# Performance work log

Hardware: AMD Instinct MI355X
Metric: run time of the kernel (lower is better)

Reference implementation:

```python
import jax, jax.numpy as jnp
import numpy as np

HEADS = 8


def setup_inputs() -> dict:
    key = jax.random.key(0)
    ks = jax.random.split(key, 5)
    B, C, H, W = 2, 256, 48, 48
    s = 0.02
    return {
        "ct": jax.random.normal(ks[0], (B, C, H, W), jnp.float32),
        "us": jax.random.normal(ks[1], (B, C, H, W), jnp.float32),
        "w_qkv_ct": jax.random.normal(ks[2], (3 * C, C), jnp.float32) * s,
        "w_qkv_us": jax.random.normal(ks[3], (3 * C, C), jnp.float32) * s,
        "w_proj": jax.random.normal(ks[4], (C, 2 * C), jnp.float32) * s,
        "b_proj": jnp.zeros((C,), jnp.float32),
    }


def _heads_view(x, B, H, W):
    # [B, C, H, W] -> [B, heads, HW, dh]
    C = x.shape[1]
    return x.reshape(B, HEADS, C // HEADS, H * W).transpose(0, 1, 3, 2)


def _cross_attn(q, k, v, scale):
    # q,k,v: [B, heads, HW, dh]
    attn = jax.nn.softmax(jnp.einsum("bhnd,bhmd->bhnm", q, k) * scale, axis=-1)
    return jnp.einsum("bhnm,bhmd->bhnd", attn, v)


def reference(ct, us, w_qkv_ct, w_qkv_us, w_proj, b_proj):
    B, C, H, W = ct.shape
    dh = C // HEADS
    scale = dh ** (-0.5)

    # 1x1 convs as channel GEMMs
    qkv1 = jnp.einsum("oc,bchw->bohw", w_qkv_ct, ct)
    qkv2 = jnp.einsum("oc,bchw->bohw", w_qkv_us, us)
    q1, k1, v1 = jnp.split(qkv1, 3, axis=1)
    q2, k2, v2 = jnp.split(qkv2, 3, axis=1)

    # CT queries attend to US keys/values
    o1 = _cross_attn(_heads_view(q1, B, H, W), _heads_view(k2, B, H, W),
                     _heads_view(v2, B, H, W), scale)
    # US queries attend to CT keys/values
    o2 = _cross_attn(_heads_view(q2, B, H, W), _heads_view(k1, B, H, W),
                     _heads_view(v1, B, H, W), scale)

    # [B, heads, HW, dh] -> [B, C, H, W]
    out1 = o1.transpose(0, 1, 3, 2).reshape(B, C, H, W)
    out2 = o2.transpose(0, 1, 3, 2).reshape(B, C, H, W)

    fused = jnp.concatenate([ct + out1, us + out2], axis=1)
    return jnp.einsum("oc,bchw->bohw", w_proj, fused) + b_proj[None, :, None, None]
```

## Files before the change

### kernel.cpp

```cpp
#include <hip/hip_runtime.h>
#include <hip/hip_bf16.h>
#include <math.h>

#define HW   2304
#define CCH  256

#define QSCALE 0.25504368686637270f

typedef short short8 __attribute__((ext_vector_type(8)));
typedef float f32x4  __attribute__((ext_vector_type(4)));

__device__ inline unsigned short f2bf(float f) {
    union { float f; unsigned u; } v; v.f = f;
    unsigned r = v.u + 0x7FFF + ((v.u >> 16) & 1);
    return (unsigned short)(r >> 16);
}
__device__ inline unsigned pkbf2(float a, float b) {
    float2 f; f.x = a; f.y = b;
    union { __hip_bfloat162 h; unsigned u; } c;
    c.h = __float22bfloat162_rn(f);
    return c.u;
}
__device__ inline unsigned pktrunc(float a, float b) {
    return __builtin_amdgcn_perm(__builtin_bit_cast(unsigned, b),
                                 __builtin_bit_cast(unsigned, a), 0x07060302u);
}


__device__ __forceinline__ void prep_unit(
    int u, int t,
    const float* __restrict__ ct, const float* __restrict__ us,
    const float* __restrict__ w1, const float* __restrict__ w2,
    const float* __restrict__ w3,
    unsigned short* __restrict__ xT,
    unsigned short* __restrict__ wb1, unsigned short* __restrict__ wb2,
    unsigned short* __restrict__ w3b,
    unsigned short* __restrict__ Ts )
{
    if (u >= 576) {
        const int v_ = u - 576;
        int z, base;
        if (v_ < 192)      { z = 0; base = v_ * 1024; }
        else if (v_ < 384) { z = 1; base = (v_ - 192) * 1024; }
        else               { z = 2; base = (v_ - 384) * 1024; }
        const float* s = (z == 0) ? w1 : (z == 1) ? w2 : w3;
        unsigned short* d = (z == 0) ? wb1 : (z == 1) ? wb2 : w3b;
        const int i = base + t * 4;
        const float4 v4 = *(const float4*)&s[i];
        const float sc = (z < 2 && i < 65536) ? QSCALE : 1.f;
        uint2 p; p.x = pkbf2(v4.x * sc, v4.y * sc); p.y = pkbf2(v4.z * sc, v4.w * sc);
        *(uint2*)&d[i] = p;
        return;
    }
    const int pt = u % 36, rest = u / 36, ctile = rest & 3, z = rest >> 2;
    const float* __restrict__ src = ((z >> 1) ? us : ct) + (size_t)(z & 1) * CCH * HW;
    unsigned short* __restrict__ dst = xT + (size_t)z * HW * 256;
    const int p0 = pt * 64, c0 = ctile * 64;
    const int m = t & 15, ms = (m & 7) << 3;
    __syncthreads();
#pragma unroll
    for (int r = 0; r < 4; r++) {
        const int c = (t >> 4) + 16 * r;
        const float4 v4 = *(const float4*)&src[(size_t)(c0 + c) * HW + p0 + m * 4];
        const int cs = c ^ ms;
        Ts[(m * 4 + 0) * 72 + cs] = f2bf(v4.x);
        Ts[(m * 4 + 1) * 72 + cs] = f2bf(v4.y);
        Ts[(m * 4 + 2) * 72 + cs] = f2bf(v4.z);
        Ts[(m * 4 + 3) * 72 + cs] = f2bf(v4.w);
    }
    __syncthreads();
    const int p = t >> 2, c8 = (t & 3) * 16;
    const int es = ((p >> 2) & 7) << 3;
    const short8 a  = *(const short8*)&Ts[p * 72 + (c8 ^ es)];
    const short8 b8 = *(const short8*)&Ts[p * 72 + ((c8 + 8) ^ es)];
    *(short8*)&dst[(size_t)(p0 + p) * 256 + c0 + c8]     = a;
    *(short8*)&dst[(size_t)(p0 + p) * 256 + c0 + c8 + 8] = b8;
}

__device__ __forceinline__ void qkv_unit(
    int ptile, int otile, int z, int t,
    const unsigned short* __restrict__ xT,
    const unsigned short* __restrict__ wb1, const unsigned short* __restrict__ wb2,
    unsigned short* __restrict__ qkvT1, unsigned short* __restrict__ qkvT2,
    unsigned short* __restrict__ vdm1,  unsigned short* __restrict__ vdm2,
    unsigned short* __restrict__ Ws, unsigned short* __restrict__ Xs)
{
    const int inp = z >> 1, b = z & 1;
    const unsigned short* __restrict__ X = xT + (size_t)(inp * 2 + b) * HW * 256;
    const unsigned short* __restrict__ W = inp ? wb2 : wb1;
    unsigned short* __restrict__ qT = (inp ? qkvT2 : qkvT1) + (size_t)b * HW * 512;
    unsigned short* __restrict__ vd = (inp ? vdm2 : vdm1) + (size_t)b * CCH * HW;
    const int p0 = ptile * 64, o0 = otile * 64;
    const int w = t >> 6, lane = t & 63, quad = lane >> 4, m = lane & 15;
    const int sr = t >> 3, sc = t & 7;

    f32x4 acc[4] = {{0,0,0,0},{0,0,0,0},{0,0,0,0},{0,0,0,0}};

    short8 wv0 = *(const short8*)&W[(size_t)(o0 + sr) * 256 + sc * 8];
    short8 wv1 = *(const short8*)&W[(size_t)(o0 + 32 + sr) * 256 + sc * 8];
    short8 xv0 = *(const short8*)&X[(size_t)(p0 + sr) * 256 + sc * 8];
    short8 xv1 = *(const short8*)&X[(size_t)(p0 + 32 + sr) * 256 + sc * 8];

    for (int k0 = 0; k0 < 256; k0 += 64) {
        __syncthreads();
        *(short8*)&Ws[sr * 72 + sc * 8] = wv0;
        *(short8*)&Ws[(32 + sr) * 72 + sc * 8] = wv1;
        *(short8*)&Xs[sr * 72 + sc * 8] = xv0;
        *(short8*)&Xs[(32 + sr) * 72 + sc * 8] = xv1;
        __syncthreads();
        const int kn = k0 + 64;
        if (kn < 256) {
            wv0 = *(const short8*)&W[(size_t)(o0 + sr) * 256 + kn + sc * 8];
            wv1 = *(const short8*)&W[(size_t)(o0 + 32 + sr) * 256 + kn + sc * 8];
            xv0 = *(const short8*)&X[(size_t)(p0 + sr) * 256 + kn + sc * 8];
            xv1 = *(const short8*)&X[(size_t)(p0 + 32 + sr) * 256 + kn + sc * 8];
        }
#pragma unroll
        for (int kc2 = 0; kc2 < 2; kc2++) {
            const short8 af = *(const short8*)&Ws[(w * 16 + m) * 72 + kc2 * 32 + quad * 8];
#pragma unroll
            for (int pg = 0; pg < 4; pg++) {
                const short8 bf = *(const short8*)&Xs[(pg * 16 + m) * 72 + kc2 * 32 + quad * 8];
                acc[pg] = __builtin_amdgcn_mfma_f32_16x16x32_bf16(af, bf, acc[pg], 0, 0, 0);
            }
        }
    }
    __syncthreads();
    if (o0 < 512) {
#pragma unroll
        for (int pg = 0; pg < 4; pg++) {
            uint2 pk; pk.x = pkbf2(acc[pg][0], acc[pg][1]); pk.y = pkbf2(acc[pg][2], acc[pg][3]);
            *(uint2*)&Ws[(pg * 16 + m) * 72 + w * 16 + quad * 4] = pk;
        }
        __syncthreads();
        const int pr = t >> 2, cc = t & 3;
        const uint4 d0 = *(const uint4*)&Ws[pr * 72 + cc * 16];
        const uint4 d1 = *(const uint4*)&Ws[pr * 72 + cc * 16 + 8];
        *(uint4*)&qT[(size_t)(p0 + pr) * 512 + o0 + cc * 16]     = d0;
        *(uint4*)&qT[(size_t)(p0 + pr) * 512 + o0 + cc * 16 + 8] = d1;
    } else {
#pragma unroll
        for (int pg = 0; pg < 4; pg++)
#pragma unroll
            for (int r = 0; r < 4; r++)
                Ws[(w * 16 + quad * 4 + r) * 72 + pg * 16 + m] = f2bf(acc[pg][r]);
        __syncthreads();
        const int dr = t >> 2, cc = t & 3;
        const uint4 d0 = *(const uint4*)&Ws[dr * 72 + cc * 16];
        const uint4 d1 = *(const uint4*)&Ws[dr * 72 + cc * 16 + 8];
        *(uint4*)&vd[(size_t)(o0 - 512 + dr) * HW + p0 + cc * 16]     = d0;
        *(uint4*)&vd[(size_t)(o0 - 512 + dr) * HW + p0 + cc * 16 + 8] = d1;
    }
    __syncthreads();
}

__device__ __forceinline__ void attn_unit(
    int ptile, int dir, int b, int h, int t,
    const unsigned short* __restrict__ qkvT1, const unsigned short* __restrict__ qkvT2,
    const unsigned short* __restrict__ vdm1,  const unsigned short* __restrict__ vdm2,
    const float* __restrict__ ct, const float* __restrict__ us,
    unsigned short* __restrict__ fusedT,
    unsigned short* __restrict__ Ks , unsigned short* __restrict__ Vs )
{
    const unsigned short* __restrict__ Qt = (dir ? qkvT2 : qkvT1) + (size_t)b * HW * 512;
    const unsigned short* __restrict__ Kt = (dir ? qkvT1 : qkvT2) + (size_t)b * HW * 512
                                            + 256 + h * 32;
    const unsigned short* __restrict__ Vd = (dir ? vdm1 : vdm2) + ((size_t)b * CCH + h * 32) * HW;
    const float* __restrict__ src = (dir ? us : ct) + ((size_t)b * CCH + h * 32) * HW;

    const int w = t >> 6, lane = t & 63, quad = lane >> 4, m = lane & 15;
    const int kj0 = t >> 2, kcs = t & 3;
    const int pcK = kcs ^ (((kj0 >> 1) & 1) | (((kj0 >> 3) & 1) << 1));
    const int vr0 = t >> 4, vcs = t & 15;
    const int g2m = ((m >> 1) & 1) | (((m >> 2) & 1) << 1);
    const unsigned short* __restrict__ ksb =
        &Ks[((m >> 2) * 8 + (m & 3)) * 32 + (quad ^ g2m) * 8];
    const unsigned short* __restrict__ vsb = &Vs[m * 136 + quad * 8];
    const short ONE = (short)0x3F80;
    const short8 ones = {ONE,ONE,ONE,ONE,ONE,ONE,ONE,ONE};

    const int pqA = ptile * 128 + w * 32 + m;
    const short8 qfA = *(const short8*)&Qt[(size_t)pqA * 512 + h * 32 + quad * 8];
    const short8 qfB = *(const short8*)&Qt[(size_t)(pqA + 16) * 512 + h * 32 + quad * 8];

    f32x4 acc0A = {0,0,0,0}, acc1A = {0,0,0,0}, acclA = {0,0,0,0};
    f32x4 acc0B = {0,0,0,0}, acc1B = {0,0,0,0}, acclB = {0,0,0,0};

    short8 ka = *(const short8*)&Kt[(size_t)kj0 * 512 + kcs * 8];
    short8 kb = *(const short8*)&Kt[(size_t)(kj0 + 64) * 512 + kcs * 8];
    short8 va = *(const short8*)&Vd[(size_t)vr0 * HW + vcs * 8];
    short8 vb = *(const short8*)&Vd[(size_t)(vr0 + 16) * HW + vcs * 8];

    for (int j0 = 0; j0 < HW; j0 += 128) {
        __syncthreads();
        *(short8*)&Ks[kj0 * 32 + pcK * 8] = ka;
        *(short8*)&Ks[(kj0 + 64) * 32 + pcK * 8] = kb;
        *(short8*)&Vs[vr0 * 136 + vcs * 8] = va;
        *(short8*)&Vs[(vr0 + 16) * 136 + vcs * 8] = vb;
        __syncthreads();

        const int jn = j0 + 128;
        if (jn < HW) {
            ka = *(const short8*)&Kt[(size_t)(jn + kj0) * 512 + kcs * 8];
            kb = *(const short8*)&Kt[(size_t)(jn + kj0 + 64) * 512 + kcs * 8];
            va = *(const short8*)&Vd[(size_t)vr0 * HW + jn + vcs * 8];
            vb = *(const short8*)&Vd[(size_t)(vr0 + 16) * HW + jn + vcs * 8];
        }

        uint4 pwA[4], pwB[4];
#pragma unroll
        for (int f = 0; f < 8; f++) {
            const short8 kf = *(const short8*)(ksb + ((f >> 1) * 32 + (f & 1) * 4) * 32);
            const f32x4 z = {0,0,0,0};
            const f32x4 SA = __builtin_amdgcn_mfma_f32_16x16x32_bf16(kf, qfA, z, 0, 0, 0);
            const f32x4 SB = __builtin_amdgcn_mfma_f32_16x16x32_bf16(kf, qfB, z, 0, 0, 0);
            const float a0 = __builtin_amdgcn_exp2f(SA[0]);
            const float a1 = __builtin_amdgcn_exp2f(SA[1]);
            const float a2 = __builtin_amdgcn_exp2f(SA[2]);
            const float a3 = __builtin_amdgcn_exp2f(SA[3]);
            const float b0 = __builtin_amdgcn_exp2f(SB[0]);
            const float b1 = __builtin_amdgcn_exp2f(SB[1]);
            const float b2 = __builtin_amdgcn_exp2f(SB[2]);
            const float b3 = __builtin_amdgcn_exp2f(SB[3]);
            if ((f & 1) == 0) {
                pwA[f >> 1].x = pktrunc(a0, a1); pwA[f >> 1].y = pktrunc(a2, a3);
                pwB[f >> 1].x = pktrunc(b0, b1); pwB[f >> 1].y = pktrunc(b2, b3);
            } else {
                pwA[f >> 1].z = pktrunc(a0, a1); pwA[f >> 1].w = pktrunc(a2, a3);
                pwB[f >> 1].z = pktrunc(b0, b1); pwB[f >> 1].w = pktrunc(b2, b3);
            }
        }
#pragma unroll
        for (int kt = 0; kt < 4; kt++) {
            const short8 pfA = __builtin_bit_cast(short8, pwA[kt]);
            const short8 pfB = __builtin_bit_cast(short8, pwB[kt]);
            const short8 vf0 = *(const short8*)(vsb + kt * 32);
            const short8 vf1 = *(const short8*)(vsb + 16 * 136 + kt * 32);
            acc0A = __builtin_amdgcn_mfma_f32_16x16x32_bf16(vf0, pfA, acc0A, 0, 0, 0);
            acc1A = __builtin_amdgcn_mfma_f32_16x16x32_bf16(vf1, pfA, acc1A, 0, 0, 0);
            acclA = __builtin_amdgcn_mfma_f32_16x16x32_bf16(ones, pfA, acclA, 0, 0, 0);
            acc0B = __builtin_amdgcn_mfma_f32_16x16x32_bf16(vf0, pfB, acc0B, 0, 0, 0);
            acc1B = __builtin_amdgcn_mfma_f32_16x16x32_bf16(vf1, pfB, acc1B, 0, 0, 0);
            acclB = __builtin_amdgcn_mfma_f32_16x16x32_bf16(ones, pfB, acclB, 0, 0, 0);
        }
    }

    const int cb = dir * 256 + h * 32, d0 = quad * 4;
    {
        const float inv = 1.f / acclA[0];
        unsigned short* __restrict__ fT = fusedT + ((size_t)b * HW + pqA) * 512 + cb + d0;
        uint2 s0, s1;
        s0.x = pkbf2(acc0A[0] * inv + src[(size_t)(d0 + 0) * HW + pqA],
                     acc0A[1] * inv + src[(size_t)(d0 + 1) * HW + pqA]);
        s0.y = pkbf2(acc0A[2] * inv + src[(size_t)(d0 + 2) * HW + pqA],
                     acc0A[3] * inv + src[(size_t)(d0 + 3) * HW + pqA]);
        s1.x = pkbf2(acc1A[0] * inv + src[(size_t)(16 + d0 + 0) * HW + pqA],
                     acc1A[1] * inv + src[(size_t)(16 + d0 + 1) * HW + pqA]);
        s1.y = pkbf2(acc1A[2] * inv + src[(size_t)(16 + d0 + 2) * HW + pqA],
                     acc1A[3] * inv + src[(size_t)(16 + d0 + 3) * HW + pqA]);
        *(uint2*)&fT[0]  = s0;
        *(uint2*)&fT[16] = s1;
    }
    {
        const int pqB = pqA + 16;
        const float inv = 1.f / acclB[0];
        unsigned short* __restrict__ fT = fusedT + ((size_t)b * HW + pqB) * 512 + cb + d0;
        uint2 s0, s1;
        s0.x = pkbf2(acc0B[0] * inv + src[(size_t)(d0 + 0) * HW + pqB],
                     acc0B[1] * inv + src[(size_t)(d0 + 1) * HW + pqB]);
        s0.y = pkbf2(acc0B[2] * inv + src[(size_t)(d0 + 2) * HW + pqB],
                     acc0B[3] * inv + src[(size_t)(d0 + 3) * HW + pqB]);
        s1.x = pkbf2(acc1B[0] * inv + src[(size_t)(16 + d0 + 0) * HW + pqB],
                     acc1B[1] * inv + src[(size_t)(16 + d0 + 1) * HW + pqB]);
        s1.y = pkbf2(acc1B[2] * inv + src[(size_t)(16 + d0 + 2) * HW + pqB],
                     acc1B[3] * inv + src[(size_t)(16 + d0 + 3) * HW + pqB]);
        *(uint2*)&fT[0]  = s0;
        *(uint2*)&fT[16] = s1;
    }
    __syncthreads();
}

__device__ __forceinline__ void proj_unit(
    int ptile, int otile, int t,
    const unsigned short* __restrict__ w3b, const unsigned short* __restrict__ fusedT,
    const float* __restrict__ bias, float* __restrict__ out,
    unsigned short* __restrict__ Ws, unsigned short* __restrict__ Xs)
{
    const int p0 = ptile * 64, o0 = otile * 64;
    const int w = t >> 6, lane = t & 63, quad = lane >> 4, m = lane & 15;
    const int sr = t >> 3, sc = t & 7;

    f32x4 acc[4] = {{0,0,0,0},{0,0,0,0},{0,0,0,0},{0,0,0,0}};

    short8 wv0 = *(const short8*)&w3b[(size_t)(o0 + sr) * 512 + sc * 8];
    short8 wv1 = *(const short8*)&w3b[(size_t)(o0 + 32 + sr) * 512 + sc * 8];
    short8 xv0 = *(const short8*)&fusedT[(size_t)(p0 + sr) * 512 + sc * 8];
    short8 xv1 = *(const short8*)&fusedT[(size_t)(p0 + 32 + sr) * 512 + sc * 8];

    for (int k0 = 0; k0 < 512; k0 += 64) {
        __syncthreads();
        *(short8*)&Ws[sr * 72 + sc * 8] = wv0;
        *(short8*)&Ws[(32 + sr) * 72 + sc * 8] = wv1;
        *(short8*)&Xs[sr * 72 + sc * 8] = xv0;
        *(short8*)&Xs[(32 + sr) * 72 + sc * 8] = xv1;
        __syncthreads();
        const int kn = k0 + 64;
        if (kn < 512) {
            wv0 = *(const short8*)&w3b[(size_t)(o0 + sr) * 512 + kn + sc * 8];
            wv1 = *(const short8*)&w3b[(size_t)(o0 + 32 + sr) * 512 + kn + sc * 8];
            xv0 = *(const short8*)&fusedT[(size_t)(p0 + sr) * 512 + kn + sc * 8];
            xv1 = *(const short8*)&fusedT[(size_t)(p0 + 32 + sr) * 512 + kn + sc * 8];
        }
#pragma unroll
        for (int kc2 = 0; kc2 < 2; kc2++) {
            const short8 af = *(const short8*)&Ws[(w * 16 + m) * 72 + kc2 * 32 + quad * 8];
#pragma unroll
            for (int pg = 0; pg < 4; pg++) {
                const short8 bf = *(const short8*)&Xs[(pg * 16 + m) * 72 + kc2 * 32 + quad * 8];
                acc[pg] = __builtin_amdgcn_mfma_f32_16x16x32_bf16(af, bf, acc[pg], 0, 0, 0);
            }
        }
    }
    const int b = (p0 >= HW) ? 1 : 0;
    const int pl0 = p0 - b * HW;
    float* __restrict__ ob = out + (size_t)b * CCH * HW;
    float b4[4];
#pragma unroll
    for (int r = 0; r < 4; r++) b4[r] = bias[o0 + w * 16 + quad * 4 + r];
#pragma unroll
    for (int pg = 0; pg < 4; pg++)
#pragma unroll
        for (int r = 0; r < 4; r++)
            ob[(size_t)(o0 + w * 16 + quad * 4 + r) * HW + pl0 + pg * 16 + m]
                = acc[pg][r] + b4[r];
}

__global__ __launch_bounds__(256, 4) void prep_k(
    const float* __restrict__ ct, const float* __restrict__ us,
    const float* __restrict__ w1, const float* __restrict__ w2,
    const float* __restrict__ w3,
    unsigned short* __restrict__ xT,
    unsigned short* __restrict__ b1, unsigned short* __restrict__ b2,
    unsigned short* __restrict__ b3)
{
    __shared__ __align__(16) unsigned short Ts[64 * 72];
    prep_unit(blockIdx.x, threadIdx.x, ct, us, w1, w2, w3, xT, b1, b2, b3, Ts);
}

__global__ __launch_bounds__(256, 4) void qkv_k(
    const unsigned short* __restrict__ xT,
    const unsigned short* __restrict__ wb1, const unsigned short* __restrict__ wb2,
    unsigned short* __restrict__ qkvT1, unsigned short* __restrict__ qkvT2,
    unsigned short* __restrict__ vdm1,  unsigned short* __restrict__ vdm2)
{
    __shared__ __align__(16) unsigned short Ws[64 * 72];
    __shared__ __align__(16) unsigned short Xs[64 * 72];
    qkv_unit(blockIdx.x, blockIdx.y, blockIdx.z, threadIdx.x,
             xT, wb1, wb2, qkvT1, qkvT2, vdm1, vdm2, Ws, Xs);
}

__global__ __launch_bounds__(256, 3) void attn_k(
    const unsigned short* __restrict__ qkvT1, const unsigned short* __restrict__ qkvT2,
    const unsigned short* __restrict__ vdm1,  const unsigned short* __restrict__ vdm2,
    const float* __restrict__ ct, const float* __restrict__ us,
    unsigned short* __restrict__ fusedT)
{
    __shared__ __align__(16) unsigned short Ks[128 * 32];
    __shared__ __align__(16) unsigned short Vs[32 * 136];
    attn_unit(blockIdx.x, blockIdx.z, blockIdx.y >> 3, blockIdx.y & 7, threadIdx.x,
              qkvT1, qkvT2, vdm1, vdm2, ct, us, fusedT, Ks, Vs);
}

__global__ __launch_bounds__(256, 4) void proj_k(
    const unsigned short* __restrict__ w3b, const unsigned short* __restrict__ fusedT,
    const float* __restrict__ bias, float* __restrict__ out)
{
    __shared__ __align__(16) unsigned short Ws[64 * 72];
    __shared__ __align__(16) unsigned short Xs[64 * 72];
    proj_unit(blockIdx.x, blockIdx.y, threadIdx.x, w3b, fusedT, bias, out, Ws, Xs);
}

extern "C" void kernel_launch(void* const* d_in, const int* in_sizes, int n_in,
                              void* d_out, int out_size, void* d_ws, size_t ws_size,
                              hipStream_t stream)
{
    const float* ct       = (const float*)d_in[0];
    const float* us       = (const float*)d_in[1];
    const float* w_qkv_ct = (const float*)d_in[2];
    const float* w_qkv_us = (const float*)d_in[3];
    const float* w_proj   = (const float*)d_in[4];
    const float* b_proj   = (const float*)d_in[5];
    float* out = (float*)d_out;

    unsigned short* wb1   = (unsigned short*)d_ws;
    unsigned short* wb2   = wb1 + (size_t)768 * 256;
    unsigned short* w3b   = wb2 + (size_t)768 * 256;
    unsigned short* xT    = w3b + (size_t)256 * 512;
    unsigned short* qkvT1 = xT    + (size_t)4 * HW * 256;
    unsigned short* qkvT2 = qkvT1 + (size_t)2 * HW * 512;
    unsigned short* vdm1  = qkvT2 + (size_t)2 * HW * 512;
    unsigned short* vdm2  = vdm1  + (size_t)2 * CCH * HW;
    unsigned short* fusedT= vdm2  + (size_t)2 * CCH * HW;

    prep_k<<<dim3(1088), 256, 0, stream>>>(ct, us, w_qkv_ct, w_qkv_us, w_proj,
                                           xT, wb1, wb2, w3b);
    qkv_k <<<dim3(36, 12, 4), 256, 0, stream>>>(xT, wb1, wb2, qkvT1, qkvT2, vdm1, vdm2);
    attn_k<<<dim3(18, 16, 2), 256, 0, stream>>>(qkvT1, qkvT2, vdm1, vdm2, ct, us, fusedT);
    proj_k<<<dim3(72, 4), 256, 0, stream>>>(w3b, fusedT, b_proj, out);
}
```

Measured before the change: 125.4 us.

## Double-buffer K/V tiles in attention and fix prep transpose swizzle

The attention kernel now keeps two LDS buffers for the K and V tiles. The next tile is written into the spare buffer while the current one is consumed, which cuts the loop from two barriers per iteration to one. The attention launch-bounds occupancy hint rises from 3 to 4 blocks per CU. The transpose in the prep kernel gets a changed XOR swizzle to reduce LDS bank conflicts. The extra buffer doubles attention LDS use, and the higher occupancy target may add register pressure or spills.

```diff
diff --git a/kernel.cpp b/kernel.cpp
--- a/kernel.cpp
+++ b/kernel.cpp
@@ -56,7 +56,7 @@
     const float* __restrict__ src = ((z >> 1) ? us : ct) + (size_t)(z & 1) * CCH * HW;
     unsigned short* __restrict__ dst = xT + (size_t)z * HW * 256;
     const int p0 = pt * 64, c0 = ctile * 64;
-    const int m = t & 15, ms = (m & 7) << 3;
+    const int m = t & 15, ms = ((m >> 1) & 7) << 3;
     __syncthreads();
 #pragma unroll
     for (int r = 0; r < 4; r++) {
@@ -70,7 +70,7 @@
     }
     __syncthreads();
     const int p = t >> 2, c8 = (t & 3) * 16;
-    const int es = ((p >> 2) & 7) << 3;
+    const int es = ((p >> 3) & 7) << 3;
     const short8 a  = *(const short8*)&Ts[p * 72 + (c8 ^ es)];
     const short8 b8 = *(const short8*)&Ts[p * 72 + ((c8 + 8) ^ es)];
     *(short8*)&dst[(size_t)(p0 + p) * 256 + c0 + c8]     = a;
@@ -154,14 +154,98 @@
     __syncthreads();
 }
 
-__device__ __forceinline__ void attn_unit(
-    int ptile, int dir, int b, int h, int t,
+__device__ __forceinline__ void proj_unit(
+    int ptile, int otile, int t,
+    const unsigned short* __restrict__ w3b, const unsigned short* __restrict__ fusedT,
+    const float* __restrict__ bias, float* __restrict__ out,
+    unsigned short* __restrict__ Ws, unsigned short* __restrict__ Xs)
+{
+    const int p0 = ptile * 64, o0 = otile * 64;
+    const int w = t >> 6, lane = t & 63, quad = lane >> 4, m = lane & 15;
+    const int sr = t >> 3, sc = t & 7;
+
+    f32x4 acc[4] = {{0,0,0,0},{0,0,0,0},{0,0,0,0},{0,0,0,0}};
+
+    short8 wv0 = *(const short8*)&w3b[(size_t)(o0 + sr) * 512 + sc * 8];
+    short8 wv1 = *(const short8*)&w3b[(size_t)(o0 + 32 + sr) * 512 + sc * 8];
+    short8 xv0 = *(const short8*)&fusedT[(size_t)(p0 + sr) * 512 + sc * 8];
+    short8 xv1 = *(const short8*)&fusedT[(size_t)(p0 + 32 + sr) * 512 + sc * 8];
+
+    for (int k0 = 0; k0 < 512; k0 += 64) {
+        __syncthreads();
+        *(short8*)&Ws[sr * 72 + sc * 8] = wv0;
+        *(short8*)&Ws[(32 + sr) * 72 + sc * 8] = wv1;
+        *(short8*)&Xs[sr * 72 + sc * 8] = xv0;
+        *(short8*)&Xs[(32 + sr) * 72 + sc * 8] = xv1;
+        __syncthreads();
+        const int kn = k0 + 64;
+        if (kn < 512) {
+            wv0 = *(const short8*)&w3b[(size_t)(o0 + sr) * 512 + kn + sc * 8];
+            wv1 = *(const short8*)&w3b[(size_t)(o0 + 32 + sr) * 512 + kn + sc * 8];
+            xv0 = *(const short8*)&fusedT[(size_t)(p0 + sr) * 512 + kn + sc * 8];
+            xv1 = *(const short8*)&fusedT[(size_t)(p0 + 32 + sr) * 512 + kn + sc * 8];
+        }
+#pragma unroll
+        for (int kc2 = 0; kc2 < 2; kc2++) {
+            const short8 af = *(const short8*)&Ws[(w * 16 + m) * 72 + kc2 * 32 + quad * 8];
+#pragma unroll
+            for (int pg = 0; pg < 4; pg++) {
+                const short8 bf = *(const short8*)&Xs[(pg * 16 + m) * 72 + kc2 * 32 + quad * 8];
+                acc[pg] = __builtin_amdgcn_mfma_f32_16x16x32_bf16(af, bf, acc[pg], 0, 0, 0);
+            }
+        }
+    }
+    const int b = (p0 >= HW) ? 1 : 0;
+    const int pl0 = p0 - b * HW;
+    float* __restrict__ ob = out + (size_t)b * CCH * HW;
+    float b4[4];
+#pragma unroll
+    for (int r = 0; r < 4; r++) b4[r] = bias[o0 + w * 16 + quad * 4 + r];
+#pragma unroll
+    for (int pg = 0; pg < 4; pg++)
+#pragma unroll
+        for (int r = 0; r < 4; r++)
+            ob[(size_t)(o0 + w * 16 + quad * 4 + r) * HW + pl0 + pg * 16 + m]
+                = acc[pg][r] + b4[r];
+}
+
+__global__ __launch_bounds__(256, 4) void prep_k(
+    const float* __restrict__ ct, const float* __restrict__ us,
+    const float* __restrict__ w1, const float* __restrict__ w2,
+    const float* __restrict__ w3,
+    unsigned short* __restrict__ xT,
+    unsigned short* __restrict__ b1, unsigned short* __restrict__ b2,
+    unsigned short* __restrict__ b3)
+{
+    __shared__ __align__(16) unsigned short Ts[64 * 72];
+    prep_unit(blockIdx.x, threadIdx.x, ct, us, w1, w2, w3, xT, b1, b2, b3, Ts);
+}
+
+__global__ __launch_bounds__(256, 4) void qkv_k(
+    const unsigned short* __restrict__ xT,
+    const unsigned short* __restrict__ wb1, const unsigned short* __restrict__ wb2,
+    unsigned short* __restrict__ qkvT1, unsigned short* __restrict__ qkvT2,
+    unsigned short* __restrict__ vdm1,  unsigned short* __restrict__ vdm2)
+{
+    __shared__ __align__(16) unsigned short Ws[64 * 72];
+    __shared__ __align__(16) unsigned short Xs[64 * 72];
+    qkv_unit(blockIdx.x, blockIdx.y, blockIdx.z, threadIdx.x,
+             xT, wb1, wb2, qkvT1, qkvT2, vdm1, vdm2, Ws, Xs);
+}
+
+__global__ __launch_bounds__(256, 4) void attn_k(
     const unsigned short* __restrict__ qkvT1, const unsigned short* __restrict__ qkvT2,
     const unsigned short* __restrict__ vdm1,  const unsigned short* __restrict__ vdm2,
     const float* __restrict__ ct, const float* __restrict__ us,
-    unsigned short* __restrict__ fusedT,
-    unsigned short* __restrict__ Ks , unsigned short* __restrict__ Vs )
-{
+    unsigned short* __restrict__ fusedT)
+{
+    __shared__ __align__(16) unsigned short Ks[2][128 * 32];
+    __shared__ __align__(16) unsigned short Vs[2][32 * 136];
+    const int t = threadIdx.x;
+
+    const int ptile = blockIdx.x, dir = blockIdx.z;
+    const int b = blockIdx.y >> 3, h = blockIdx.y & 7;
+
     const unsigned short* __restrict__ Qt = (dir ? qkvT2 : qkvT1) + (size_t)b * HW * 512;
     const unsigned short* __restrict__ Kt = (dir ? qkvT1 : qkvT2) + (size_t)b * HW * 512
                                             + 256 + h * 32;
@@ -173,9 +257,8 @@
     const int pcK = kcs ^ (((kj0 >> 1) & 1) | (((kj0 >> 3) & 1) << 1));
     const int vr0 = t >> 4, vcs = t & 15;
     const int g2m = ((m >> 1) & 1) | (((m >> 2) & 1) << 1);
-    const unsigned short* __restrict__ ksb =
-        &Ks[((m >> 2) * 8 + (m & 3)) * 32 + (quad ^ g2m) * 8];
-    const unsigned short* __restrict__ vsb = &Vs[m * 136 + quad * 8];
+    const int ksb_off = ((m >> 2) * 8 + (m & 3)) * 32 + (quad ^ g2m) * 8;
+    const int vsb_off = m * 136 + quad * 8;
     const short ONE = (short)0x3F80;
     const short8 ones = {ONE,ONE,ONE,ONE,ONE,ONE,ONE,ONE};
 
@@ -190,22 +273,34 @@
     short8 kb = *(const short8*)&Kt[(size_t)(kj0 + 64) * 512 + kcs * 8];
     short8 va = *(const short8*)&Vd[(size_t)vr0 * HW + vcs * 8];
     short8 vb = *(const short8*)&Vd[(size_t)(vr0 + 16) * HW + vcs * 8];
-
-    for (int j0 = 0; j0 < HW; j0 += 128) {
-        __syncthreads();
-        *(short8*)&Ks[kj0 * 32 + pcK * 8] = ka;
-        *(short8*)&Ks[(kj0 + 64) * 32 + pcK * 8] = kb;
-        *(short8*)&Vs[vr0 * 136 + vcs * 8] = va;
-        *(short8*)&Vs[(vr0 + 16) * 136 + vcs * 8] = vb;
-        __syncthreads();
-
-        const int jn = j0 + 128;
+    *(short8*)&Ks[0][kj0 * 32 + pcK * 8] = ka;
+    *(short8*)&Ks[0][(kj0 + 64) * 32 + pcK * 8] = kb;
+    *(short8*)&Vs[0][vr0 * 136 + vcs * 8] = va;
+    *(short8*)&Vs[0][(vr0 + 16) * 136 + vcs * 8] = vb;
+    ka = *(const short8*)&Kt[(size_t)(128 + kj0) * 512 + kcs * 8];
+    kb = *(const short8*)&Kt[(size_t)(128 + kj0 + 64) * 512 + kcs * 8];
+    va = *(const short8*)&Vd[(size_t)vr0 * HW + 128 + vcs * 8];
+    vb = *(const short8*)&Vd[(size_t)(vr0 + 16) * HW + 128 + vcs * 8];
+    __syncthreads();
+
+    for (int ti = 0; ti < 18; ti++) {
+        const int cur = ti & 1, nxt = cur ^ 1;
+        if (ti < 17) {
+            *(short8*)&Ks[nxt][kj0 * 32 + pcK * 8] = ka;
+            *(short8*)&Ks[nxt][(kj0 + 64) * 32 + pcK * 8] = kb;
+            *(short8*)&Vs[nxt][vr0 * 136 + vcs * 8] = va;
+            *(short8*)&Vs[nxt][(vr0 + 16) * 136 + vcs * 8] = vb;
+        }
+        const int jn = (ti + 2) * 128;
         if (jn < HW) {
             ka = *(const short8*)&Kt[(size_t)(jn + kj0) * 512 + kcs * 8];
             kb = *(const short8*)&Kt[(size_t)(jn + kj0 + 64) * 512 + kcs * 8];
             va = *(const short8*)&Vd[(size_t)vr0 * HW + jn + vcs * 8];
             vb = *(const short8*)&Vd[(size_t)(vr0 + 16) * HW + jn + vcs * 8];
         }
+
+        const unsigned short* __restrict__ ksb = &Ks[cur][ksb_off];
+        const unsigned short* __restrict__ vsb = &Vs[cur][vsb_off];
 
         uint4 pwA[4], pwB[4];
 #pragma unroll
@@ -243,6 +338,7 @@
             acc1B = __builtin_amdgcn_mfma_f32_16x16x32_bf16(vf1, pfB, acc1B, 0, 0, 0);
             acclB = __builtin_amdgcn_mfma_f32_16x16x32_bf16(ones, pfB, acclB, 0, 0, 0);
         }
+        __syncthreads();
     }
 
     const int cb = dir * 256 + h * 32, d0 = quad * 4;
@@ -277,98 +373,6 @@
         *(uint2*)&fT[0]  = s0;
         *(uint2*)&fT[16] = s1;
     }
-    __syncthreads();
-}
-
-__device__ __forceinline__ void proj_unit(
-    int ptile, int otile, int t,
-    const unsigned short* __restrict__ w3b, const unsigned short* __restrict__ fusedT,
-    const float* __restrict__ bias, float* __restrict__ out,
-    unsigned short* __restrict__ Ws, unsigned short* __restrict__ Xs)
-{
-    const int p0 = ptile * 64, o0 = otile * 64;
-    const int w = t >> 6, lane = t & 63, quad = lane >> 4, m = lane & 15;
-    const int sr = t >> 3, sc = t & 7;
-
-    f32x4 acc[4] = {{0,0,0,0},{0,0,0,0},{0,0,0,0},{0,0,0,0}};
-
-    short8 wv0 = *(const short8*)&w3b[(size_t)(o0 + sr) * 512 + sc * 8];
-    short8 wv1 = *(const short8*)&w3b[(size_t)(o0 + 32 + sr) * 512 + sc * 8];
-    short8 xv0 = *(const short8*)&fusedT[(size_t)(p0 + sr) * 512 + sc * 8];
-    short8 xv1 = *(const short8*)&fusedT[(size_t)(p0 + 32 + sr) * 512 + sc * 8];
-
-    for (int k0 = 0; k0 < 512; k0 += 64) {
-        __syncthreads();
-        *(short8*)&Ws[sr * 72 + sc * 8] = wv0;
-        *(short8*)&Ws[(32 + sr) * 72 + sc * 8] = wv1;
-        *(short8*)&Xs[sr * 72 + sc * 8] = xv0;
-        *(short8*)&Xs[(32 + sr) * 72 + sc * 8] = xv1;
-        __syncthreads();
-        const int kn = k0 + 64;
-        if (kn < 512) {
-            wv0 = *(const short8*)&w3b[(size_t)(o0 + sr) * 512 + kn + sc * 8];
-            wv1 = *(const short8*)&w3b[(size_t)(o0 + 32 + sr) * 512 + kn + sc * 8];
-            xv0 = *(const short8*)&fusedT[(size_t)(p0 + sr) * 512 + kn + sc * 8];
-            xv1 = *(const short8*)&fusedT[(size_t)(p0 + 32 + sr) * 512 + kn + sc * 8];
-        }
-#pragma unroll
-        for (int kc2 = 0; kc2 < 2; kc2++) {
-            const short8 af = *(const short8*)&Ws[(w * 16 + m) * 72 + kc2 * 32 + quad * 8];
-#pragma unroll
-            for (int pg = 0; pg < 4; pg++) {
-                const short8 bf = *(const short8*)&Xs[(pg * 16 + m) * 72 + kc2 * 32 + quad * 8];
-                acc[pg] = __builtin_amdgcn_mfma_f32_16x16x32_bf16(af, bf, acc[pg], 0, 0, 0);
-            }
-        }
-    }
-    const int b = (p0 >= HW) ? 1 : 0;
-    const int pl0 = p0 - b * HW;
-    float* __restrict__ ob = out + (size_t)b * CCH * HW;
-    float b4[4];
-#pragma unroll
-    for (int r = 0; r < 4; r++) b4[r] = bias[o0 + w * 16 + quad * 4 + r];
-#pragma unroll
-    for (int pg = 0; pg < 4; pg++)
-#pragma unroll
-        for (int r = 0; r < 4; r++)
-            ob[(size_t)(o0 + w * 16 + quad * 4 + r) * HW + pl0 + pg * 16 + m]
-                = acc[pg][r] + b4[r];
-}
-
-__global__ __launch_bounds__(256, 4) void prep_k(
-    const float* __restrict__ ct, const float* __restrict__ us,
-    const float* __restrict__ w1, const float* __restrict__ w2,
-    const float* __restrict__ w3,
-    unsigned short* __restrict__ xT,
-    unsigned short* __restrict__ b1, unsigned short* __restrict__ b2,
-    unsigned short* __restrict__ b3)
-{
-    __shared__ __align__(16) unsigned short Ts[64 * 72];
-    prep_unit(blockIdx.x, threadIdx.x, ct, us, w1, w2, w3, xT, b1, b2, b3, Ts);
-}
-
-__global__ __launch_bounds__(256, 4) void qkv_k(
-    const unsigned short* __restrict__ xT,
-    const unsigned short* __restrict__ wb1, const unsigned short* __restrict__ wb2,
-    unsigned short* __restrict__ qkvT1, unsigned short* __restrict__ qkvT2,
-    unsigned short* __restrict__ vdm1,  unsigned short* __restrict__ vdm2)
-{
-    __shared__ __align__(16) unsigned short Ws[64 * 72];
-    __shared__ __align__(16) unsigned short Xs[64 * 72];
-    qkv_unit(blockIdx.x, blockIdx.y, blockIdx.z, threadIdx.x,
-             xT, wb1, wb2, qkvT1, qkvT2, vdm1, vdm2, Ws, Xs);
-}
-
-__global__ __launch_bounds__(256, 3) void attn_k(
-    const unsigned short* __restrict__ qkvT1, const unsigned short* __restrict__ qkvT2,
-    const unsigned short* __restrict__ vdm1,  const unsigned short* __restrict__ vdm2,
-    const float* __restrict__ ct, const float* __restrict__ us,
-    unsigned short* __restrict__ fusedT)
-{
-    __shared__ __align__(16) unsigned short Ks[128 * 32];
-    __shared__ __align__(16) unsigned short Vs[32 * 136];
-    attn_unit(blockIdx.x, blockIdx.z, blockIdx.y >> 3, blockIdx.y & 7, threadIdx.x,
-              qkvT1, qkvT2, vdm1, vdm2, ct, us, fusedT, Ks, Vs);
 }
 
 __global__ __launch_bounds__(256, 4) void proj_k(
```

Result: slower. 128.9 us (+2.8%).
